# Kernel tuning notes

Measured on AMD Instinct MI355X. Metric: run time of the kernel, lower is better.

## Reference

```python
import jax, jax.numpy as jnp
import numpy as np

T, B, N, DIN, H = 64, 32, 64, 128, 128  # seq_len, batch, num_nodes, input_dim, hid_dim
NUM_LAYERS = 2


def _make_cell_params(key, din):
    k1, k2, k3, k4 = jax.random.split(key, 4)
    s = 0.05
    Wg = jax.random.normal(k1, (2 * (din + H), 2 * H), jnp.float32) * s  # gates (r,u)
    bg = jnp.zeros((2 * H,), jnp.float32)
    Wc = jax.random.normal(k2, (2 * (din + H), H), jnp.float32) * s      # candidate
    bc = jnp.zeros((H,), jnp.float32)
    Wq = jax.random.normal(k3, (H, H), jnp.float32) * s                  # graph learner q
    Wk = jax.random.normal(k4, (H, H), jnp.float32) * s                  # graph learner k
    return Wg, bg, Wc, bc, Wq, Wk


def setup_inputs() -> dict:
    key = jax.random.key(0)
    k_in, k_sup, k_l0, k_l1 = jax.random.split(key, 4)
    inputs = jax.random.normal(k_in, (T, B, N, DIN), jnp.float32)
    initial_hidden_state = jnp.zeros((NUM_LAYERS, B, N * H), jnp.float32)
    supports = jax.nn.softmax(jax.random.normal(k_sup, (B, N, N), jnp.float32), axis=-1)
    Wg0, bg0, Wc0, bc0, Wq0, Wk0 = _make_cell_params(k_l0, DIN)
    Wg1, bg1, Wc1, bc1, Wq1, Wk1 = _make_cell_params(k_l1, H)
    return dict(inputs=inputs, initial_hidden_state=initial_hidden_state, supports=supports,
                Wg0=Wg0, bg0=bg0, Wc0=Wc0, bc0=bc0, Wq0=Wq0, Wk0=Wk0,
                Wg1=Wg1, bg1=bg1, Wc1=Wc1, bc1=bc1, Wq1=Wq1, Wk1=Wk1)


def _cell_step(params, supports, x, h):
    # x: (B, N, din), h: (B, N, H), supports: (B, N, N)
    Wg, bg, Wc, bc, Wq, Wk = params
    xh = jnp.concatenate([x, h], axis=-1)
    conv = jnp.einsum('bnm,bmd->bnd', supports, xh)                # graph conv
    gates = jax.nn.sigmoid(jnp.concatenate([xh, conv], -1) @ Wg + bg)
    r, u = jnp.split(gates, 2, axis=-1)
    xh_r = jnp.concatenate([x, r * h], axis=-1)
    conv_c = jnp.einsum('bnm,bmd->bnd', supports, xh_r)
    c = jnp.tanh(jnp.concatenate([xh_r, conv_c], -1) @ Wc + bc)
    h_new = u * h + (1.0 - u) * c
    # dynamic graph learner: new adjacency from the updated hidden state
    scores = jnp.einsum('bnd,bmd->bnm', h_new @ Wq, h_new @ Wk)
    new_supports = jax.nn.softmax(jax.nn.relu(scores), axis=-1)
    return h_new, new_supports


def _run_layer(params, x_seq, h0, supports, din):
    # x_seq: (T, B, N*din) -> hidden sequence (T, B, N, H)
    def step(carry, x_t):
        h, sup = carry
        h_new, sup_new = _cell_step(params, sup, x_t.reshape(B, N, din), h)
        return (h_new, sup_new), h_new
    (h_last, sup_last), hs = jax.lax.scan(step, (h0.reshape(B, N, H), supports), x_seq)
    return hs, h_last, sup_last


def reference(inputs, initial_hidden_state, supports,
              Wg0, bg0, Wc0, bc0, Wq0, Wk0,
              Wg1, bg1, Wc1, bc1, Wq1, Wk1):
    layer_params = [(Wg0, bg0, Wc0, bc0, Wq0, Wk0), (Wg1, bg1, Wc1, bc1, Wq1, Wk1)]
    dins = [DIN, H]
    cur = inputs.reshape(T, B, N * DIN)
    sup = supports
    out_hidden = []
    for i in range(NUM_LAYERS):
        hs, h_last, sup = _run_layer(layer_params[i], cur, initial_hidden_state[i], sup, dins[i])
        out_hidden.append(h_last.reshape(B, N * H))
        cur = hs.reshape(T, B, N * H)
    output_hidden = jnp.stack(out_hidden, axis=0)   # (num_layers, B, N*H)
    return output_hidden, cur                        # cur: (T, B, N*H)
```

## Files before the change

### kernel.cpp

```cpp
#include <hip/hip_runtime.h>

#define TT 64
#define BB 32
#define NN 64
#define HH 128
#define NH 8192

using short8 = __attribute__((ext_vector_type(8))) short;
using f32x16 = __attribute__((ext_vector_type(16))) float;

__device__ __forceinline__ unsigned short f2bf(float f) {
  unsigned int u = __float_as_uint(f);
  u = (u + 0x7FFFu + ((u >> 16) & 1u)) >> 16;
  return (unsigned short)u;
}
__device__ __forceinline__ float bf2f(unsigned short s) {
  return __uint_as_float(((unsigned int)s) << 16);
}
__device__ __forceinline__ float sigm(float x) { return 1.0f / (1.0f + __expf(-x)); }
__device__ __forceinline__ float tanh_fast(float x) { return 2.0f / (1.0f + __expf(-2.0f * x)) - 1.0f; }

__device__ __forceinline__ uint2 pack4(float a, float b, float c, float d) {
  uint2 r;
  r.x = (unsigned int)f2bf(a) | ((unsigned int)f2bf(b) << 16);
  r.y = (unsigned int)f2bf(c) | ((unsigned int)f2bf(d) << 16);
  return r;
}
__device__ __forceinline__ short8 ldsfrag(const unsigned short* p) {
  union { uint2 u2[2]; short8 s; } f;
  f.u2[0] = *(const uint2*)p;
  f.u2[1] = *(const uint2*)(p + 4);
  return f.s;
}
__device__ __forceinline__ short8 ldgfrag(const unsigned short* p) {
  union { uint4 u4; short8 s; } f;
  f.u4 = *(const uint4*)p;
  return f.s;
}

__global__ void sglc_pack(const float* __restrict__ Wg0, const float* __restrict__ Wc0,
                          const float* __restrict__ Wq0, const float* __restrict__ Wk0,
                          const float* __restrict__ Wg1, const float* __restrict__ Wc1,
                          const float* __restrict__ Wq1, const float* __restrict__ Wk1,
                          unsigned short* __restrict__ dst) {
  int idx = blockIdx.x * 256 + threadIdx.x;
  if (idx >= 458752) return;
  int layer = idx / 229376;
  int lo = idx - layer * 229376;
  const float* src; int nkc, ncshift, off;
  if (lo < 131072)      { src = layer ? Wg1 : Wg0; nkc = 32; ncshift = 8; off = 0; }
  else if (lo < 196608) { src = layer ? Wc1 : Wc0; nkc = 32; ncshift = 7; off = 131072; }
  else if (lo < 212992) { src = layer ? Wq1 : Wq0; nkc = 8;  ncshift = 7; off = 196608; }
  else                  { src = layer ? Wk1 : Wk0; nkc = 8;  ncshift = 7; off = 212992; }
  int l2 = lo - off;
  int k = l2 >> ncshift;
  int c = l2 & ((1 << ncshift) - 1);
  int c32 = c >> 5, n32 = c & 31;
  int kc = k >> 4, kl = k & 15;
  int half = kl >> 3, j = kl & 7;
  int lane = half * 32 + n32;
  int dstoff = layer * 229376 + off + (((c32 * nkc + kc) << 9) + lane * 8 + j);
  dst[dstoff] = f2bf(src[(size_t)k * (1 << ncshift) + c]);
}

#define SX_O   0
#define SH_O   8448
#define SRH_O  16896
#define SQ_O   25344
#define SK_O   33792
#define SSUP_O 42240
#define SPT_O  46592
#define LDS_USHORTS 64000
#define SHF_BYTES 32768
#define LDS_BYTES (LDS_USHORTS * 2 + SHF_BYTES)

extern "C" __global__ void __launch_bounds__(1024, 4)
sglc_main(const float* __restrict__ Xin, const float* __restrict__ H0,
          const float* __restrict__ Sup0,
          const float* __restrict__ bg0, const float* __restrict__ bc0,
          const float* __restrict__ bg1, const float* __restrict__ bc1,
          const unsigned short* __restrict__ Wp, float* __restrict__ Out) {
  extern __shared__ unsigned short sm[];
  unsigned short* sX   = sm + SX_O;
  unsigned short* sHb  = sm + SH_O;
  unsigned short* sRH  = sm + SRH_O;
  unsigned short* sQ   = sm + SQ_O;
  unsigned short* sK   = sm + SK_O;
  unsigned short* sSup = sm + SSUP_O;
  unsigned short* sPT  = sm + SPT_O;
  float* sS  = (float*)(sm + SPT_O);
  float* uS  = (float*)(sm + SQ_O);
  float* sHf = (float*)(sm + LDS_USHORTS);

  const int b = blockIdx.x;
  const int tid = threadIdx.x;
  const int lane = tid & 63;
  const int w = tid >> 6;
  const int n32 = lane & 31;
  const int half = lane >> 5;
  const int kob = half * 8;

  float* OutH = Out;
  float* Cur  = Out + 2 * BB * NH;

  for (int layer = 0; layer < 2; ++layer) {
    const int Lw = layer * 229376;
    const float* bg = layer ? bg1 : bg0;
    const float* bc = layer ? bc1 : bc0;
    const float* xbase = layer ? Cur : Xin;
    const float* h0p = H0 + (size_t)(layer * BB + b) * NH;

    const float bgv = (w < 8) ? bg[(w & 7) * 32 + n32] : 0.0f;
    const float bcv = (w >= 4 && w < 8) ? bc[(w - 4) * 32 + n32] : 0.0f;

    {
      int r = tid >> 4, c0 = (tid & 15) * 8;
      const float* hp = h0p + r * 128 + c0;
      float4 v0 = *(const float4*)(hp);
      float4 v1 = *(const float4*)(hp + 4);
      *(uint2*)(sHb + r * 132 + c0)     = pack4(v0.x, v0.y, v0.z, v0.w);
      *(uint2*)(sHb + r * 132 + c0 + 4) = pack4(v1.x, v1.y, v1.z, v1.w);
      *(float4*)(sHf + r * 128 + c0)     = v0;
      *(float4*)(sHf + r * 128 + c0 + 4) = v1;
      const float* xp = xbase + (size_t)(0 * BB + b) * NH + r * 128 + c0;
      float4 x0 = *(const float4*)(xp);
      float4 x1 = *(const float4*)(xp + 4);
      *(uint2*)(sX + r * 132 + c0)     = pack4(x0.x, x0.y, x0.z, x0.w);
      *(uint2*)(sX + r * 132 + c0 + 4) = pack4(x1.x, x1.y, x1.z, x1.w);
      if (layer == 0) {
        int rs = tid >> 4, cs = (tid & 15) * 4;
        float4 sv = *(const float4*)(Sup0 + (size_t)b * 4096 + rs * 64 + cs);
        *(uint2*)(sSup + rs * 68 + cs) = pack4(sv.x, sv.y, sv.z, sv.w);
      }
    }
    __syncthreads();

    for (int t = 0; t < TT; ++t) {
      f32x16 acc0, acc1;
#pragma unroll
      for (int z = 0; z < 16; ++z) { acc0[z] = 0.0f; acc1[z] = 0.0f; }

      {
        const int c32g = w & 7;
        const unsigned short* wb = Wp + Lw + (((c32g * 32 + (w < 8 ? 0 : 16)) << 9) + lane * 8);
#pragma unroll
        for (int kc = 0; kc < 16; ++kc) {
          const unsigned short* asrc = (kc < 8) ? (sX + kc * 16 + kob) : (sHb + (kc - 8) * 16 + kob);
          short8 a0 = ldsfrag(asrc + n32 * 132);
          short8 a1 = ldsfrag(asrc + (32 + n32) * 132);
          short8 bf = ldgfrag(wb + (kc << 9));
          acc0 = __builtin_amdgcn_mfma_f32_32x32x16_bf16(a0, bf, acc0, 0, 0, 0);
          acc1 = __builtin_amdgcn_mfma_f32_32x32x16_bf16(a1, bf, acc1, 0, 0, 0);
        }
        if (w >= 8) {
          unsigned short* pb = sPT + (c32g * 32 + n32) * 68;
#pragma unroll
          for (int tt = 0; tt < 2; ++tt) {
            const f32x16& ac = tt ? acc1 : acc0;
#pragma unroll
            for (int g = 0; g < 4; ++g)
              *(uint2*)(pb + tt * 32 + 8 * g + 4 * half) =
                  pack4(ac[4 * g], ac[4 * g + 1], ac[4 * g + 2], ac[4 * g + 3]);
          }
        }
      }
      __syncthreads();

      if (w < 8) {
        const int c32g = w & 7;
#pragma unroll
        for (int kc2 = 0; kc2 < 4; ++kc2) {
          short8 a0 = ldsfrag(sSup + n32 * 68 + kc2 * 16 + kob);
          short8 a1 = ldsfrag(sSup + (32 + n32) * 68 + kc2 * 16 + kob);
          short8 bf = ldsfrag(sPT + (c32g * 32 + n32) * 68 + kc2 * 16 + kob);
          acc0 = __builtin_amdgcn_mfma_f32_32x32x16_bf16(a0, bf, acc0, 0, 0, 0);
          acc1 = __builtin_amdgcn_mfma_f32_32x32x16_bf16(a1, bf, acc1, 0, 0, 0);
        }
        if (w < 4) {
          const int col = (w & 7) * 32 + n32;
#pragma unroll
          for (int tt = 0; tt < 2; ++tt) {
            const f32x16& ac = tt ? acc1 : acc0;
#pragma unroll
            for (int g = 0; g < 4; ++g)
#pragma unroll
              for (int i = 0; i < 4; ++i) {
                int row = tt * 32 + 8 * g + 4 * half + i;
                float rv = sigm(ac[4 * g + i] + bgv);
                float hv = bf2f(sHb[row * 132 + col]);
                sRH[row * 132 + col] = f2bf(rv * hv);
              }
          }
        } else {
          const int ucol = (w - 4) * 32 + n32;
#pragma unroll
          for (int tt = 0; tt < 2; ++tt) {
            const f32x16& ac = tt ? acc1 : acc0;
#pragma unroll
            for (int g = 0; g < 4; ++g)
#pragma unroll
              for (int i = 0; i < 4; ++i) {
                int row = tt * 32 + 8 * g + 4 * half + i;
                uS[row * 128 + ucol] = sigm(ac[4 * g + i] + bgv);
              }
          }
        }
      }
      __syncthreads();

      f32x16 ca0, ca1;
#pragma unroll
      for (int z = 0; z < 16; ++z) { ca0[z] = 0.0f; ca1[z] = 0.0f; }
      if (w >= 4 && w < 12) {
        const int c32c = (w < 8) ? (w - 4) : (w - 8);
        const unsigned short* wb = Wp + Lw + 131072 + (((c32c * 32 + (w < 8 ? 0 : 16)) << 9) + lane * 8);
#pragma unroll
        for (int kc = 0; kc < 16; ++kc) {
          const unsigned short* asrc = (kc < 8) ? (sX + kc * 16 + kob) : (sRH + (kc - 8) * 16 + kob);
          short8 a0 = ldsfrag(asrc + n32 * 132);
          short8 a1 = ldsfrag(asrc + (32 + n32) * 132);
          short8 bf = ldgfrag(wb + (kc << 9));
          ca0 = __builtin_amdgcn_mfma_f32_32x32x16_bf16(a0, bf, ca0, 0, 0, 0);
          ca1 = __builtin_amdgcn_mfma_f32_32x32x16_bf16(a1, bf, ca1, 0, 0, 0);
        }
        if (w >= 8) {
          unsigned short* pb = sPT + (c32c * 32 + n32) * 68;
#pragma unroll
          for (int tt = 0; tt < 2; ++tt) {
            const f32x16& ac = tt ? ca1 : ca0;
#pragma unroll
            for (int g = 0; g < 4; ++g)
              *(uint2*)(pb + tt * 32 + 8 * g + 4 * half) =
                  pack4(ac[4 * g], ac[4 * g + 1], ac[4 * g + 2], ac[4 * g + 3]);
          }
        }
      }
      __syncthreads();

      if (w >= 4 && w < 8) {
        const int c32c = w - 4;
        const int col = c32c * 32 + n32;
#pragma unroll
        for (int kc2 = 0; kc2 < 4; ++kc2) {
          short8 a0 = ldsfrag(sSup + n32 * 68 + kc2 * 16 + kob);
          short8 a1 = ldsfrag(sSup + (32 + n32) * 68 + kc2 * 16 + kob);
          short8 bf = ldsfrag(sPT + col * 68 + kc2 * 16 + kob);
          ca0 = __builtin_amdgcn_mfma_f32_32x32x16_bf16(a0, bf, ca0, 0, 0, 0);
          ca1 = __builtin_amdgcn_mfma_f32_32x32x16_bf16(a1, bf, ca1, 0, 0, 0);
        }
        float* curp = Cur + (size_t)(t * BB + b) * NH;
#pragma unroll
        for (int tt = 0; tt < 2; ++tt) {
          const f32x16& ac = tt ? ca1 : ca0;
#pragma unroll
          for (int g = 0; g < 4; ++g)
#pragma unroll
            for (int i = 0; i < 4; ++i) {
              int row = tt * 32 + 8 * g + 4 * half + i;
              float cv = tanh_fast(ac[4 * g + i] + bcv);
              float uv = uS[row * 128 + col];
              float hold = sHf[row * 128 + col];
              float hn = uv * hold + (1.0f - uv) * cv;
              sHf[row * 128 + col] = hn;
              sHb[row * 132 + col] = f2bf(hn);
              curp[row * 128 + col] = hn;
            }
        }
      } else if (w < 4 || w >= 12) {
        if (t < TT - 1) {
          const float* xn = xbase + (size_t)((t + 1) * BB + b) * NH;
          int sidx = (w < 4 ? w : w - 8) * 64 + lane;
          int r = sidx >> 3, c0 = (sidx & 7) * 16;
          const float* sp = xn + r * 128 + c0;
          unsigned short* dp = sX + r * 132 + c0;
#pragma unroll
          for (int q4 = 0; q4 < 4; ++q4) {
            float4 v = *(const float4*)(sp + q4 * 4);
            *(uint2*)(dp + q4 * 4) = pack4(v.x, v.y, v.z, v.w);
          }
        }
      }
      __syncthreads();

      if (w >= 8) {
        const unsigned short* qb =
            Wp + Lw + ((w < 12) ? 196608 : 212992) + ((((w - 8) & 3) * 8) << 9) + lane * 8;
        const int col = ((w - 8) & 3) * 32 + n32;
        f32x16 qa0, qa1;
#pragma unroll
        for (int z = 0; z < 16; ++z) { qa0[z] = 0.0f; qa1[z] = 0.0f; }
#pragma unroll
        for (int kc = 0; kc < 8; ++kc) {
          short8 a0 = ldsfrag(sHb + n32 * 132 + kc * 16 + kob);
          short8 a1 = ldsfrag(sHb + (32 + n32) * 132 + kc * 16 + kob);
          short8 bf = ldgfrag(qb + (kc << 9));
          qa0 = __builtin_amdgcn_mfma_f32_32x32x16_bf16(a0, bf, qa0, 0, 0, 0);
          qa1 = __builtin_amdgcn_mfma_f32_32x32x16_bf16(a1, bf, qa1, 0, 0, 0);
        }
        unsigned short* dstm = (w < 12) ? sQ : sK;
#pragma unroll
        for (int tt = 0; tt < 2; ++tt) {
          const f32x16& ac = tt ? qa1 : qa0;
#pragma unroll
          for (int g = 0; g < 4; ++g)
#pragma unroll
            for (int i = 0; i < 4; ++i)
              dstm[(tt * 32 + 8 * g + 4 * half + i) * 132 + col] = f2bf(ac[4 * g + i]);
        }
      }
      __syncthreads();

      if (w < 4) {
        const int rt = w & 1, ct = w >> 1;
        f32x16 sa;
#pragma unroll
        for (int z = 0; z < 16; ++z) sa[z] = 0.0f;
#pragma unroll
        for (int kc = 0; kc < 8; ++kc) {
          short8 a0 = ldsfrag(sQ + (rt * 32 + n32) * 132 + kc * 16 + kob);
          short8 bf = ldsfrag(sK + (ct * 32 + n32) * 132 + kc * 16 + kob);
          sa = __builtin_amdgcn_mfma_f32_32x32x16_bf16(a0, bf, sa, 0, 0, 0);
        }
#pragma unroll
        for (int g = 0; g < 4; ++g)
#pragma unroll
          for (int i = 0; i < 4; ++i)
            sS[(rt * 32 + 8 * g + 4 * half + i) * 66 + ct * 32 + n32] = fmaxf(sa[4 * g + i], 0.0f);
      }
      __syncthreads();

      {
        int row = tid >> 4, ci = (tid & 15) * 4;
        float2 v01 = *(const float2*)(sS + row * 66 + ci);
        float2 v23 = *(const float2*)(sS + row * 66 + ci + 2);
        float s0 = v01.x, s1 = v01.y, s2 = v23.x, s3 = v23.y;
        float mx = fmaxf(fmaxf(s0, s1), fmaxf(s2, s3));
#pragma unroll
        for (int off = 1; off < 16; off <<= 1) mx = fmaxf(mx, __shfl_xor(mx, off, 16));
        float e0 = __expf(s0 - mx), e1 = __expf(s1 - mx);
        float e2 = __expf(s2 - mx), e3 = __expf(s3 - mx);
        float sum = e0 + e1 + e2 + e3;
#pragma unroll
        for (int off = 1; off < 16; off <<= 1) sum += __shfl_xor(sum, off, 16);
        float inv = 1.0f / sum;
        *(uint2*)(sSup + row * 68 + ci) = pack4(e0 * inv, e1 * inv, e2 * inv, e3 * inv);
      }
      __syncthreads();
    }

    {
      float* outp = OutH + (size_t)(layer * BB + b) * NH;
      int r = tid >> 4, c0 = (tid & 15) * 8;
      *(float4*)(outp + r * 128 + c0)     = *(const float4*)(sHf + r * 128 + c0);
      *(float4*)(outp + r * 128 + c0 + 4) = *(const float4*)(sHf + r * 128 + c0 + 4);
    }
    __syncthreads();
  }
}

extern "C" void kernel_launch(void* const* d_in, const int* in_sizes, int n_in,
                              void* d_out, int out_size, void* d_ws, size_t ws_size,
                              hipStream_t stream) {
  const float* Xin  = (const float*)d_in[0];
  const float* H0   = (const float*)d_in[1];
  const float* Sup0 = (const float*)d_in[2];
  const float* Wg0  = (const float*)d_in[3];
  const float* bg0  = (const float*)d_in[4];
  const float* Wc0  = (const float*)d_in[5];
  const float* bc0  = (const float*)d_in[6];
  const float* Wq0  = (const float*)d_in[7];
  const float* Wk0  = (const float*)d_in[8];
  const float* Wg1  = (const float*)d_in[9];
  const float* bg1  = (const float*)d_in[10];
  const float* Wc1  = (const float*)d_in[11];
  const float* bc1  = (const float*)d_in[12];
  const float* Wq1  = (const float*)d_in[13];
  const float* Wk1  = (const float*)d_in[14];
  unsigned short* Wp = (unsigned short*)d_ws;

  hipFuncSetAttribute(reinterpret_cast<const void*>(sglc_main),
                      hipFuncAttributeMaxDynamicSharedMemorySize, LDS_BYTES);

  hipLaunchKernelGGL(sglc_pack, dim3(1792), dim3(256), 0, stream,
                     Wg0, Wc0, Wq0, Wk0, Wg1, Wc1, Wq1, Wk1, Wp);
  hipLaunchKernelGGL(sglc_main, dim3(BB), dim3(1024), LDS_BYTES, stream,
                     Xin, H0, Sup0, bg0, bc0, bg1, bc1, Wp, (float*)d_out);
}
```

Before: 3.087 ms.

## Precompute Wq·Wkᵀ product so graph scores need one projection per step

A new pre-kernel computes M = Wq·Wkᵀ for each layer and stores it in bf16 in the packed weight slot. The main loop then computes only (h·M) and takes scores = (h·M)·hᵀ against the bf16 hidden state, which removes the separate K projection and its LDS buffer. The projection work is spread over 8 waves, each handling one 32-row tile. Accumulator registers are now shared across phases, and r·h reads the fp32 hidden copy instead of the bf16 one. Rounding changes because M is formed in fp32 and then quantized to bf16.

```diff
diff --git a/kernel.cpp b/kernel.cpp
--- a/kernel.cpp
+++ b/kernel.cpp
@@ -63,6 +63,31 @@
   dst[dstoff] = f2bf(src[(size_t)k * (1 << ncshift) + c]);
 }
 
+__global__ void sglc_packM(const float* __restrict__ Wq0, const float* __restrict__ Wk0,
+                           const float* __restrict__ Wq1, const float* __restrict__ Wk1,
+                           unsigned short* __restrict__ dst) {
+  int idx = blockIdx.x * 256 + threadIdx.x;
+  int layer = idx >> 14;
+  int off = idx & 16383;
+  int block = off >> 9;
+  int lane = (off >> 3) & 63;
+  int j = off & 7;
+  int c32 = block >> 3, kc = block & 7;
+  int half = lane >> 5, n32 = lane & 31;
+  int a = kc * 16 + half * 8 + j;
+  int bcol = c32 * 32 + n32;
+  const float* Q = layer ? Wq1 : Wq0;
+  const float* K = layer ? Wk1 : Wk0;
+  float s = 0.0f;
+#pragma unroll 4
+  for (int e = 0; e < 128; e += 4) {
+    float4 qa = *(const float4*)(Q + a * 128 + e);
+    float4 kb = *(const float4*)(K + bcol * 128 + e);
+    s += qa.x * kb.x + qa.y * kb.y + qa.z * kb.z + qa.w * kb.w;
+  }
+  dst[layer * 229376 + 196608 + (block << 9) + lane * 8 + j] = f2bf(s);
+}
+
 #define SX_O   0
 #define SH_O   8448
 #define SRH_O  16896
@@ -85,7 +110,6 @@
   unsigned short* sHb  = sm + SH_O;
   unsigned short* sRH  = sm + SRH_O;
   unsigned short* sQ   = sm + SQ_O;
-  unsigned short* sK   = sm + SK_O;
   unsigned short* sSup = sm + SSUP_O;
   unsigned short* sPT  = sm + SPT_O;
   float* sS  = (float*)(sm + SPT_O);
@@ -136,9 +160,9 @@
     __syncthreads();
 
     for (int t = 0; t < TT; ++t) {
-      f32x16 acc0, acc1;
-#pragma unroll
-      for (int z = 0; z < 16; ++z) { acc0[z] = 0.0f; acc1[z] = 0.0f; }
+      f32x16 A0, A1;
+#pragma unroll
+      for (int z = 0; z < 16; ++z) { A0[z] = 0.0f; A1[z] = 0.0f; }
 
       {
         const int c32g = w & 7;
@@ -149,14 +173,14 @@
           short8 a0 = ldsfrag(asrc + n32 * 132);
           short8 a1 = ldsfrag(asrc + (32 + n32) * 132);
           short8 bf = ldgfrag(wb + (kc << 9));
-          acc0 = __builtin_amdgcn_mfma_f32_32x32x16_bf16(a0, bf, acc0, 0, 0, 0);
-          acc1 = __builtin_amdgcn_mfma_f32_32x32x16_bf16(a1, bf, acc1, 0, 0, 0);
+          A0 = __builtin_amdgcn_mfma_f32_32x32x16_bf16(a0, bf, A0, 0, 0, 0);
+          A1 = __builtin_amdgcn_mfma_f32_32x32x16_bf16(a1, bf, A1, 0, 0, 0);
         }
         if (w >= 8) {
           unsigned short* pb = sPT + (c32g * 32 + n32) * 68;
 #pragma unroll
           for (int tt = 0; tt < 2; ++tt) {
-            const f32x16& ac = tt ? acc1 : acc0;
+            const f32x16& ac = tt ? A1 : A0;
 #pragma unroll
             for (int g = 0; g < 4; ++g)
               *(uint2*)(pb + tt * 32 + 8 * g + 4 * half) =
@@ -173,21 +197,21 @@
           short8 a0 = ldsfrag(sSup + n32 * 68 + kc2 * 16 + kob);
           short8 a1 = ldsfrag(sSup + (32 + n32) * 68 + kc2 * 16 + kob);
           short8 bf = ldsfrag(sPT + (c32g * 32 + n32) * 68 + kc2 * 16 + kob);
-          acc0 = __builtin_amdgcn_mfma_f32_32x32x16_bf16(a0, bf, acc0, 0, 0, 0);
-          acc1 = __builtin_amdgcn_mfma_f32_32x32x16_bf16(a1, bf, acc1, 0, 0, 0);
+          A0 = __builtin_amdgcn_mfma_f32_32x32x16_bf16(a0, bf, A0, 0, 0, 0);
+          A1 = __builtin_amdgcn_mfma_f32_32x32x16_bf16(a1, bf, A1, 0, 0, 0);
         }
         if (w < 4) {
           const int col = (w & 7) * 32 + n32;
 #pragma unroll
           for (int tt = 0; tt < 2; ++tt) {
-            const f32x16& ac = tt ? acc1 : acc0;
+            const f32x16& ac = tt ? A1 : A0;
 #pragma unroll
             for (int g = 0; g < 4; ++g)
 #pragma unroll
               for (int i = 0; i < 4; ++i) {
                 int row = tt * 32 + 8 * g + 4 * half + i;
                 float rv = sigm(ac[4 * g + i] + bgv);
-                float hv = bf2f(sHb[row * 132 + col]);
+                float hv = sHf[row * 128 + col];
                 sRH[row * 132 + col] = f2bf(rv * hv);
               }
           }
@@ -195,7 +219,7 @@
           const int ucol = (w - 4) * 32 + n32;
 #pragma unroll
           for (int tt = 0; tt < 2; ++tt) {
-            const f32x16& ac = tt ? acc1 : acc0;
+            const f32x16& ac = tt ? A1 : A0;
 #pragma unroll
             for (int g = 0; g < 4; ++g)
 #pragma unroll
@@ -208,10 +232,9 @@
       }
       __syncthreads();
 
-      f32x16 ca0, ca1;
-#pragma unroll
-      for (int z = 0; z < 16; ++z) { ca0[z] = 0.0f; ca1[z] = 0.0f; }
       if (w >= 4 && w < 12) {
+#pragma unroll
+        for (int z = 0; z < 16; ++z) { A0[z] = 0.0f; A1[z] = 0.0f; }
         const int c32c = (w < 8) ? (w - 4) : (w - 8);
         const unsigned short* wb = Wp + Lw + 131072 + (((c32c * 32 + (w < 8 ? 0 : 16)) << 9) + lane * 8);
 #pragma unroll
@@ -220,14 +243,14 @@
           short8 a0 = ldsfrag(asrc + n32 * 132);
           short8 a1 = ldsfrag(asrc + (32 + n32) * 132);
           short8 bf = ldgfrag(wb + (kc << 9));
-          ca0 = __builtin_amdgcn_mfma_f32_32x32x16_bf16(a0, bf, ca0, 0, 0, 0);
-          ca1 = __builtin_amdgcn_mfma_f32_32x32x16_bf16(a1, bf, ca1, 0, 0, 0);
+          A0 = __builtin_amdgcn_mfma_f32_32x32x16_bf16(a0, bf, A0, 0, 0, 0);
+          A1 = __builtin_amdgcn_mfma_f32_32x32x16_bf16(a1, bf, A1, 0, 0, 0);
         }
         if (w >= 8) {
           unsigned short* pb = sPT + (c32c * 32 + n32) * 68;
 #pragma unroll
           for (int tt = 0; tt < 2; ++tt) {
-            const f32x16& ac = tt ? ca1 : ca0;
+            const f32x16& ac = tt ? A1 : A0;
 #pragma unroll
             for (int g = 0; g < 4; ++g)
               *(uint2*)(pb + tt * 32 + 8 * g + 4 * half) =
@@ -245,13 +268,13 @@
           short8 a0 = ldsfrag(sSup + n32 * 68 + kc2 * 16 + kob);
           short8 a1 = ldsfrag(sSup + (32 + n32) * 68 + kc2 * 16 + kob);
           short8 bf = ldsfrag(sPT + col * 68 + kc2 * 16 + kob);
-          ca0 = __builtin_amdgcn_mfma_f32_32x32x16_bf16(a0, bf, ca0, 0, 0, 0);
-          ca1 = __builtin_amdgcn_mfma_f32_32x32x16_bf16(a1, bf, ca1, 0, 0, 0);
+          A0 = __builtin_amdgcn_mfma_f32_32x32x16_bf16(a0, bf, A0, 0, 0, 0);
+          A1 = __builtin_amdgcn_mfma_f32_32x32x16_bf16(a1, bf, A1, 0, 0, 0);
         }
         float* curp = Cur + (size_t)(t * BB + b) * NH;
 #pragma unroll
         for (int tt = 0; tt < 2; ++tt) {
-          const f32x16& ac = tt ? ca1 : ca0;
+          const f32x16& ac = tt ? A1 : A0;
 #pragma unroll
           for (int g = 0; g < 4; ++g)
 #pragma unroll
@@ -283,49 +306,41 @@
       __syncthreads();
 
       if (w >= 8) {
-        const unsigned short* qb =
-            Wp + Lw + ((w < 12) ? 196608 : 212992) + ((((w - 8) & 3) * 8) << 9) + lane * 8;
-        const int col = ((w - 8) & 3) * 32 + n32;
-        f32x16 qa0, qa1;
-#pragma unroll
-        for (int z = 0; z < 16; ++z) { qa0[z] = 0.0f; qa1[z] = 0.0f; }
+        const int rt5 = (w - 8) >> 2;
+        const int c32q = (w - 8) & 3;
+        const unsigned short* qb = Wp + Lw + 196608 + (((c32q * 8) << 9) + lane * 8);
+#pragma unroll
+        for (int z = 0; z < 16; ++z) A0[z] = 0.0f;
 #pragma unroll
         for (int kc = 0; kc < 8; ++kc) {
-          short8 a0 = ldsfrag(sHb + n32 * 132 + kc * 16 + kob);
-          short8 a1 = ldsfrag(sHb + (32 + n32) * 132 + kc * 16 + kob);
+          short8 a0 = ldsfrag(sHb + (rt5 * 32 + n32) * 132 + kc * 16 + kob);
           short8 bf = ldgfrag(qb + (kc << 9));
-          qa0 = __builtin_amdgcn_mfma_f32_32x32x16_bf16(a0, bf, qa0, 0, 0, 0);
-          qa1 = __builtin_amdgcn_mfma_f32_32x32x16_bf16(a1, bf, qa1, 0, 0, 0);
-        }
-        unsigned short* dstm = (w < 12) ? sQ : sK;
-#pragma unroll
-        for (int tt = 0; tt < 2; ++tt) {
-          const f32x16& ac = tt ? qa1 : qa0;
-#pragma unroll
-          for (int g = 0; g < 4; ++g)
-#pragma unroll
-            for (int i = 0; i < 4; ++i)
-              dstm[(tt * 32 + 8 * g + 4 * half + i) * 132 + col] = f2bf(ac[4 * g + i]);
-        }
+          A0 = __builtin_amdgcn_mfma_f32_32x32x16_bf16(a0, bf, A0, 0, 0, 0);
+        }
+        const int col = c32q * 32 + n32;
+#pragma unroll
+        for (int g = 0; g < 4; ++g)
+#pragma unroll
+          for (int i = 0; i < 4; ++i)
+            sQ[(rt5 * 32 + 8 * g + 4 * half + i) * 132 + col] = f2bf(A0[4 * g + i]);
       }
       __syncthreads();
 
       if (w < 4) {
         const int rt = w & 1, ct = w >> 1;
-        f32x16 sa;
-#pragma unroll
-        for (int z = 0; z < 16; ++z) sa[z] = 0.0f;
+#pragma unroll
+        for (int z = 0; z < 16; ++z) A0[z] = 0.0f;
 #pragma unroll
         for (int kc = 0; kc < 8; ++kc) {
           short8 a0 = ldsfrag(sQ + (rt * 32 + n32) * 132 + kc * 16 + kob);
-          short8 bf = ldsfrag(sK + (ct * 32 + n32) * 132 + kc * 16 + kob);
-          sa = __builtin_amdgcn_mfma_f32_32x32x16_bf16(a0, bf, sa, 0, 0, 0);
+          short8 bf = ldsfrag(sHb + (ct * 32 + n32) * 132 + kc * 16 + kob);
+          A0 = __builtin_amdgcn_mfma_f32_32x32x16_bf16(a0, bf, A0, 0, 0, 0);
         }
 #pragma unroll
         for (int g = 0; g < 4; ++g)
 #pragma unroll
           for (int i = 0; i < 4; ++i)
-            sS[(rt * 32 + 8 * g + 4 * half + i) * 66 + ct * 32 + n32] = fmaxf(sa[4 * g + i], 0.0f);
+            sS[(rt * 32 + 8 * g + 4 * half + i) * 66 + ct * 32 + n32] = fmaxf(A0[4 * g + i], 0.0f);
       }
       __syncthreads();
 
@@ -383,6 +398,8 @@
 
   hipLaunchKernelGGL(sglc_pack, dim3(1792), dim3(256), 0, stream,
                      Wg0, Wc0, Wq0, Wk0, Wg1, Wc1, Wq1, Wk1, Wp);
+  hipLaunchKernelGGL(sglc_packM, dim3(128), dim3(256), 0, stream,
+                     Wq0, Wk0, Wq1, Wk1, Wp);
   hipLaunchKernelGGL(sglc_main, dim3(BB), dim3(1024), LDS_BYTES, stream,
                      Xin, H0, Sup0, bg0, bc0, bg1, bc1, Wp, (float*)d_out);
 }
```

Result: slower. 3.605 ms (+16.8%).
